# Kernel optimization log

Measured on AMD Instinct MI355X. Metric: run time of the kernel, lower is better.

Reference implementation:

```python
import jax, jax.numpy as jnp
import numpy as np


def setup_inputs() -> dict:
    key = jax.random.key(0)
    k1_key, k2_key = jax.random.split(key)
    C_OUT, C_IN, NB, K = 64, 64, 4, 15
    k1 = jax.random.normal(k1_key, (C_OUT * NB, C_IN * NB, K, K), dtype=jnp.float32)
    k2 = jax.random.normal(k2_key, (C_OUT * NB, C_IN * NB, K, K), dtype=jnp.float32)
    return {"k1": k1, "k2": k2, "n_blades": NB}


def _blade_conv(x, w):
    # x: [nb, nb, K, K] treated as NCHW batch, w: [nb, nb, K, K] treated as OIHW filter
    return jax.lax.conv(x, w, window_strides=(1, 1), padding="SAME")


def reference(k1, k2, n_blades):
    A, B, K, _ = k1.shape
    co, ci = A // n_blades, B // n_blades
    # (co*nb, ci*nb, K, K) -> (co, ci, nb, nb, K, K)
    a = k1.reshape(co, n_blades, ci, n_blades, K, K).transpose(0, 2, 1, 3, 4, 5)
    b = k2.reshape(co, n_blades, ci, n_blades, K, K).transpose(0, 2, 1, 3, 4, 5)
    # double vmap over (co, ci): each is a tiny nb x nb SAME conv
    k = jax.vmap(jax.vmap(_blade_conv))(a, b)  # (co, ci, nb, nb, K, K)
    k = k.transpose(0, 2, 1, 3, 4, 5).reshape(co * n_blades, ci * n_blades, K, K)
    return k
```

## Files before the change

### kernel.cpp

```cpp
#include <hip/hip_runtime.h>


typedef float f32x4 __attribute__((ext_vector_type(4)));
typedef __bf16 bf16x8 __attribute__((ext_vector_type(8)));

#define KS 15
#define SP 225
#define NCH 256
#define RSTRIDE 56
#define ROWS 183
#define APAD_SHORTS (ROWS * RSTRIDE)
#define TBL_OFF (APAD_SHORTS * 2)
#define TBL_UPC 496
#define ARENA_B (TBL_OFF + 4 * TBL_UPC * 8)

__device__ __forceinline__ unsigned short f2bf(float f) {
    unsigned u = __builtin_bit_cast(unsigned, f);
    u += 0x7FFFu + ((u >> 16) & 1u);
    return (unsigned short)(u >> 16);
}

__global__ __launch_bounds__(512, 6)
void blade_conv_mfma(const float* __restrict__ k1,
                     const float* __restrict__ k2,
                     float* __restrict__ out) {
    __shared__ __align__(16) unsigned char arena[ARENA_B];
    unsigned short*     Apad  = (unsigned short*)arena;
    unsigned long long* tbl   = (unsigned long long*)(arena + TBL_OFF);
    float*              slabs = (float*)arena;

    const int tid  = threadIdx.x;
    const int lane = tid & 63;
    const int wid  = tid >> 6;
    const int c_w  = wid & 3;
    const int np   = wid >> 2;
    const int co = blockIdx.x, ci = blockIdx.y;

    f32x4 z = {0.f, 0.f, 0.f, 0.f};
    for (int i = tid; i < ARENA_B / 16; i += 512) ((f32x4*)arena)[i] = z;
    __syncthreads();

    {
        const int lo = tid & 255, half = tid >> 8;
        if (lo < 225) {
            const int y = lo / 15, x = lo - y * 15;
            #pragma unroll
            for (int j = 0; j < 8; ++j) {
                int n = 2 * half + (j >> 2), cc = j & 3;
                float v = k1[((size_t)((co * 4 + n) * NCH + ci * 4 + cc)) * SP + lo];
                int band = n * 2 + (cc >> 1), side = cc & 1;
                Apad[(band * 22 + 7 + y) * RSTRIDE + side * 24 + 7 + x] = f2bf(v);
            }
            #pragma unroll
            for (int jj = 0; jj < 2; ++jj) {
                int cc = 2 * half + jj;
                size_t base = ((size_t)(co * 4) * NCH + ci * 4 + cc) * SP + lo;
                float v0 = k2[base];
                float v1 = k2[base + (size_t)NCH * SP];
                float v2 = k2[base + 2 * (size_t)NCH * SP];
                float v3 = k2[base + 3 * (size_t)NCH * SP];
                unsigned lw = (unsigned)f2bf(v0) | ((unsigned)f2bf(v1) << 16);
                unsigned hw = (unsigned)f2bf(v2) | ((unsigned)f2bf(v3) << 16);
                tbl[cc * TBL_UPC + 32 * y + x + 15] =
                    (unsigned long long)lw | ((unsigned long long)hw << 32);
            }
        }
    }
    __syncthreads();

    f32x4 acc[2][4];
    #pragma unroll
    for (int g = 0; g < 2; ++g)
        #pragma unroll
        for (int o = 0; o < 4; ++o)
            acc[g][o] = z;

    const int yl    = lane & 15;
    const int kg    = lane >> 4;
    const int side_w = c_w & 1, whalf = c_w >> 1;
    const int acol  = side_w * 24 + (kg << 3);
    const unsigned long long* tbase =
        &tbl[c_w * TBL_UPC + (kg << 3) - yl + 15];

    #pragma unroll
    for (int ky = 0; ky < 15; ++ky) {
        bf16x8 af[2];
        #pragma unroll
        for (int g = 0; g < 2; ++g) {
            int band = (2 * np + g) * 2 + whalf;
            af[g] = *(const bf16x8*)&Apad[(band * 22 + yl + ky) * RSTRIDE + acol];
        }
        unsigned long long q[8];
        #pragma unroll
        for (int j = 0; j < 8; ++j) q[j] = tbase[32 * ky + j];

        union { bf16x8 v; unsigned u[4]; } bo0, bo1, bo2, bo3;
        #pragma unroll
        for (int t = 0; t < 4; ++t) {
            unsigned a0 = (unsigned)q[2 * t],         a1 = (unsigned)q[2 * t + 1];
            unsigned b0 = (unsigned)(q[2 * t] >> 32), b1 = (unsigned)(q[2 * t + 1] >> 32);
            bo0.u[t] = __builtin_amdgcn_perm(a1, a0, 0x05040100u);
            bo1.u[t] = __builtin_amdgcn_perm(a1, a0, 0x07060302u);
            bo2.u[t] = __builtin_amdgcn_perm(b1, b0, 0x05040100u);
            bo3.u[t] = __builtin_amdgcn_perm(b1, b0, 0x07060302u);
        }
        #pragma unroll
        for (int g = 0; g < 2; ++g) {
            acc[g][0] = __builtin_amdgcn_mfma_f32_16x16x32_bf16(af[g], bo0.v, acc[g][0], 0, 0, 0);
            acc[g][1] = __builtin_amdgcn_mfma_f32_16x16x32_bf16(af[g], bo1.v, acc[g][1], 0, 0, 0);
            acc[g][2] = __builtin_amdgcn_mfma_f32_16x16x32_bf16(af[g], bo2.v, acc[g][2], 0, 0, 0);
            acc[g][3] = __builtin_amdgcn_mfma_f32_16x16x32_bf16(af[g], bo3.v, acc[g][3], 0, 0, 0);
        }
    }

    const int xl = lane & 15;
    #pragma unroll
    for (int r = 0; r < 4; ++r) {
        const int g = r >> 1, op = r & 1;
        __syncthreads();
        {
            float* slab = slabs + wid * 640;
            #pragma unroll
            for (int oi = 0; oi < 2; ++oi)
                *(f32x4*)&slab[(oi * 16 + xl) * 20 + (kg << 2)] = acc[g][2 * op + oi];
        }
        __syncthreads();
        for (int idx = tid; idx < 900; idx += 512) {
            int q4 = idx / 225;
            int rem = idx - q4 * 225;
            int np_g = q4 >> 1, oi = q4 & 1;
            int yy = rem / 15, xx = rem - yy * 15;
            int soff = (oi * 16 + xx) * 20 + yy;
            const float* sb = slabs + np_g * 2560;
            float s = sb[soff] + sb[640 + soff] + sb[1280 + soff] + sb[1920 + soff];
            int n = 2 * np_g + g, o = 2 * op + oi;
            out[((size_t)((co * 4 + n) * NCH + ci * 4 + o)) * SP + rem] = s;
        }
    }
}

extern "C" void kernel_launch(void* const* d_in, const int* in_sizes, int n_in,
                              void* d_out, int out_size, void* d_ws, size_t ws_size,
                              hipStream_t stream) {
    (void)in_sizes; (void)n_in; (void)d_ws; (void)ws_size; (void)out_size;
    const float* k1 = (const float*)d_in[0];
    const float* k2 = (const float*)d_in[1];
    float* out = (float*)d_out;

    dim3 grid(64, 64, 1);
    dim3 block(512, 1, 1);
    hipLaunchKernelGGL(blade_conv_mfma, grid, block, 0, stream, k1, k2, out);
}
```

Baseline: 77.58 us.

## Pre-pair k2 taps into split LDS tables to drop in-loop perm shuffles

```diff
diff --git a/kernel.cpp b/kernel.cpp
--- a/kernel.cpp
+++ b/kernel.cpp
@@ -11,8 +11,9 @@
 #define ROWS 183
 #define APAD_SHORTS (ROWS * RSTRIDE)
 #define TBL_OFF (APAD_SHORTS * 2)
-#define TBL_UPC 496
-#define ARENA_B (TBL_OFF + 4 * TBL_UPC * 8)
+#define TBL_UPC 512
+#define TBL_BYTES (4 * TBL_UPC * 8)
+#define ARENA_B (TBL_OFF + 2 * TBL_BYTES)
 
 __device__ __forceinline__ unsigned short f2bf(float f) {
     unsigned u = __builtin_bit_cast(unsigned, f);
@@ -26,7 +27,8 @@
                      float* __restrict__ out) {
     __shared__ __align__(16) unsigned char arena[ARENA_B];
     unsigned short*     Apad  = (unsigned short*)arena;
-    unsigned long long* tbl   = (unsigned long long*)(arena + TBL_OFF);
+    unsigned long long* tbl01 = (unsigned long long*)(arena + TBL_OFF);
+    unsigned long long* tbl23 = tbl01 + 4 * TBL_UPC;
     float*              slabs = (float*)arena;
 
     const int tid  = threadIdx.x;
@@ -51,20 +53,28 @@
                 int band = n * 2 + (cc >> 1), side = cc & 1;
                 Apad[(band * 22 + 7 + y) * RSTRIDE + side * 24 + 7 + x] = f2bf(v);
             }
-            #pragma unroll
-            for (int jj = 0; jj < 2; ++jj) {
-                int cc = 2 * half + jj;
-                size_t base = ((size_t)(co * 4) * NCH + ci * 4 + cc) * SP + lo;
-                float v0 = k2[base];
-                float v1 = k2[base + (size_t)NCH * SP];
-                float v2 = k2[base + 2 * (size_t)NCH * SP];
-                float v3 = k2[base + 3 * (size_t)NCH * SP];
-                unsigned lw = (unsigned)f2bf(v0) | ((unsigned)f2bf(v1) << 16);
-                unsigned hw = (unsigned)f2bf(v2) | ((unsigned)f2bf(v3) << 16);
-                tbl[cc * TBL_UPC + 32 * y + x + 15] =
-                    (unsigned long long)lw | ((unsigned long long)hw << 32);
-            }
         }
+    }
+
+    for (int idx = tid; idx < 960; idx += 512) {
+        int cc  = idx / 240;
+        int rem = idx - cc * 240;
+        int ky  = rem >> 4, si = rem & 15;
+        size_t b0 = ((size_t)(co * 4) * NCH + ci * 4 + cc) * SP + ky * KS;
+        float e0[4], e1[4];
+        #pragma unroll
+        for (int o = 0; o < 4; ++o) {
+            size_t bo = b0 + (size_t)o * NCH * SP;
+            e0[o] = (si >= 1)  ? k2[bo + si - 1] : 0.f;
+            e1[o] = (si <= 14) ? k2[bo + si]     : 0.f;
+        }
+        unsigned l01 = (unsigned)f2bf(e0[0]) | ((unsigned)f2bf(e1[0]) << 16);
+        unsigned h01 = (unsigned)f2bf(e0[1]) | ((unsigned)f2bf(e1[1]) << 16);
+        unsigned l23 = (unsigned)f2bf(e0[2]) | ((unsigned)f2bf(e1[2]) << 16);
+        unsigned h23 = (unsigned)f2bf(e0[3]) | ((unsigned)f2bf(e1[3]) << 16);
+        int u = cc * TBL_UPC + 33 * ky + 14 + si;
+        tbl01[u] = (unsigned long long)l01 | ((unsigned long long)h01 << 32);
+        tbl23[u] = (unsigned long long)l23 | ((unsigned long long)h23 << 32);
     }
     __syncthreads();
 
@@ -79,38 +89,35 @@
     const int kg    = lane >> 4;
     const int side_w = c_w & 1, whalf = c_w >> 1;
     const int acol  = side_w * 24 + (kg << 3);
-    const unsigned long long* tbase =
-        &tbl[c_w * TBL_UPC + (kg << 3) - yl + 15];
+    const int ubase = (kg << 3) - yl + 15;
+    const unsigned* tb01 = (const unsigned*)(tbl01 + c_w * TBL_UPC + ubase);
+    const unsigned* tb23 = (const unsigned*)(tbl23 + c_w * TBL_UPC + ubase);
+    const unsigned short* ab0 =
+        &Apad[(((2 * np + 0) * 2 + whalf) * 22 + yl) * RSTRIDE + acol];
+    const unsigned short* ab1 =
+        &Apad[(((2 * np + 1) * 2 + whalf) * 22 + yl) * RSTRIDE + acol];
 
     #pragma unroll
     for (int ky = 0; ky < 15; ++ky) {
-        bf16x8 af[2];
-        #pragma unroll
-        for (int g = 0; g < 2; ++g) {
-            int band = (2 * np + g) * 2 + whalf;
-            af[g] = *(const bf16x8*)&Apad[(band * 22 + yl + ky) * RSTRIDE + acol];
-        }
-        unsigned long long q[8];
-        #pragma unroll
-        for (int j = 0; j < 8; ++j) q[j] = tbase[32 * ky + j];
+        bf16x8 af0 = *(const bf16x8*)(ab0 + ky * RSTRIDE);
+        bf16x8 af1 = *(const bf16x8*)(ab1 + ky * RSTRIDE);
 
         union { bf16x8 v; unsigned u[4]; } bo0, bo1, bo2, bo3;
         #pragma unroll
         for (int t = 0; t < 4; ++t) {
-            unsigned a0 = (unsigned)q[2 * t],         a1 = (unsigned)q[2 * t + 1];
-            unsigned b0 = (unsigned)(q[2 * t] >> 32), b1 = (unsigned)(q[2 * t + 1] >> 32);
-            bo0.u[t] = __builtin_amdgcn_perm(a1, a0, 0x05040100u);
-            bo1.u[t] = __builtin_amdgcn_perm(a1, a0, 0x07060302u);
-            bo2.u[t] = __builtin_amdgcn_perm(b1, b0, 0x05040100u);
-            bo3.u[t] = __builtin_amdgcn_perm(b1, b0, 0x07060302u);
+            bo0.u[t] = tb01[66 * ky + 4 * t];
+            bo1.u[t] = tb01[66 * ky + 4 * t + 1];
+            bo2.u[t] = tb23[66 * ky + 4 * t];
+            bo3.u[t] = tb23[66 * ky + 4 * t + 1];
         }
-        #pragma unroll
-        for (int g = 0; g < 2; ++g) {
-            acc[g][0] = __builtin_amdgcn_mfma_f32_16x16x32_bf16(af[g], bo0.v, acc[g][0], 0, 0, 0);
-            acc[g][1] = __builtin_amdgcn_mfma_f32_16x16x32_bf16(af[g], bo1.v, acc[g][1], 0, 0, 0);
-            acc[g][2] = __builtin_amdgcn_mfma_f32_16x16x32_bf16(af[g], bo2.v, acc[g][2], 0, 0, 0);
-            acc[g][3] = __builtin_amdgcn_mfma_f32_16x16x32_bf16(af[g], bo3.v, acc[g][3], 0, 0, 0);
-        }
+        acc[0][0] = __builtin_amdgcn_mfma_f32_16x16x32_bf16(af0, bo0.v, acc[0][0], 0, 0, 0);
+        acc[0][1] = __builtin_amdgcn_mfma_f32_16x16x32_bf16(af0, bo1.v, acc[0][1], 0, 0, 0);
+        acc[0][2] = __builtin_amdgcn_mfma_f32_16x16x32_bf16(af0, bo2.v, acc[0][2], 0, 0, 0);
+        acc[0][3] = __builtin_amdgcn_mfma_f32_16x16x32_bf16(af0, bo3.v, acc[0][3], 0, 0, 0);
+        acc[1][0] = __builtin_amdgcn_mfma_f32_16x16x32_bf16(af1, bo0.v, acc[1][0], 0, 0, 0);
+        acc[1][1] = __builtin_amdgcn_mfma_f32_16x16x32_bf16(af1, bo1.v, acc[1][1], 0, 0, 0);
+        acc[1][2] = __builtin_amdgcn_mfma_f32_16x16x32_bf16(af1, bo2.v, acc[1][2], 0, 0, 0);
+        acc[1][3] = __builtin_amdgcn_mfma_f32_16x16x32_bf16(af1, bo3.v, acc[1][3], 0, 0, 0);
     }
 
     const int xl = lane & 15;
```

Result: no change. 78.09 us (+0.7%).
